# Kernel optimization log

Hardware: AMD Instinct MI355X
Metric: run time of the kernel (lower is better)

## Reference

```python
import jax, jax.numpy as jnp
import numpy as np

B, S, H, V, A = 64, 512, 1024, 32000, 16
MAX_LEN = 2 * 512 + 2  # 2*TEST_SEQ_LENGTH + 2


def setup_inputs() -> dict:
    key = jax.random.key(0)
    ks = jax.random.split(key, 8)
    sc_h = 1.0 / np.sqrt(H)
    return {
        "x": jax.random.randint(ks[0], (B, S), 0, V),
        "true_actions": jax.random.randint(ks[1], (B, S), 0, A),
        "true_states": jax.random.randint(ks[2], (B, S), 0, A),
        "use_forcing": 0,
        "embed_tok": jax.random.normal(ks[3], (V, H), jnp.float32) * 0.02,
        "embed_pos": jax.random.normal(ks[4], (MAX_LEN, H), jnp.float32) * 0.02,
        "Wi": jax.random.normal(ks[5], (H, 4 * H), jnp.float32) * sc_h,
        "Wh": jax.random.normal(ks[6], (H, 4 * H), jnp.float32) * sc_h,
        "bh": jnp.zeros((4 * H,), jnp.float32),
        "Wd": jax.random.normal(ks[7], (H, A), jnp.float32) * sc_h,
        "bd": jnp.zeros((A,), jnp.float32),
    }


def reference(x, true_actions, true_states, use_forcing,
              embed_tok, embed_pos, Wi, Wh, bh, Wd, bd):
    batch, seq = x.shape
    # token + positional embedding
    xe = embed_tok[x] + embed_pos[jnp.arange(seq)][None, :, :]  # [B,S,H]
    # precompute input contribution to all gates (hoisted out of the scan)
    xi = jnp.einsum('bsh,hg->bsg', xe, Wi)  # [B,S,4H]

    def step(carry, xt):
        c, h = carry
        z = xt + h @ Wh + bh                      # [B,4H]
        i, f, g, o = jnp.split(z, 4, axis=-1)     # flax gate order i,f,g,o
        c = jax.nn.sigmoid(f) * c + jax.nn.sigmoid(i) * jnp.tanh(g)
        h = jax.nn.sigmoid(o) * jnp.tanh(c)
        return (c, h), h

    c0 = jnp.zeros((batch, H), xi.dtype)
    h0 = jnp.zeros((batch, H), xi.dtype)
    _, hs = jax.lax.scan(step, (c0, h0), jnp.swapaxes(xi, 0, 1))  # [S,B,H]
    hs = jnp.swapaxes(hs, 0, 1)  # [B,S,H]

    logits_buf = hs @ Wd + bd  # [B,S,A]
    dummy = jnp.zeros((batch, seq, 1), logits_buf.dtype)
    return (dummy, logits_buf, dummy)
```

## Files before the change

kernel.cpp:

```cpp
#include <hip/hip_runtime.h>
#include <hip/hip_bf16.h>

#define BB 64
#define SS 512
#define HH 1024
#define G4 4096

using bf8_t = __attribute__((ext_vector_type(8))) short;
using f32x4 = __attribute__((ext_vector_type(4))) float;
typedef unsigned long long ull;

__device__ inline ushort f2bf(float f) {
  __hip_bfloat16 h = __float2bfloat16(f);
  return *reinterpret_cast<ushort*>(&h);
}
__device__ inline float bf2f(ushort u) {
  unsigned v = ((unsigned)u) << 16;
  return __uint_as_float(v);
}

__global__ __launch_bounds__(256) void k_transpose_cast(
    const float* __restrict__ in, ushort* __restrict__ out, int R, int C) {
  __shared__ float tile[32][33];
  int c0 = blockIdx.x * 32, r0 = blockIdx.y * 32;
  int tx = threadIdx.x & 31, ty = threadIdx.x >> 5;
  for (int i = ty; i < 32; i += 8) {
    int r = r0 + i, c = c0 + tx;
    tile[i][tx] = (r < R && c < C) ? in[(size_t)r * C + c] : 0.f;
  }
  __syncthreads();
  for (int i = ty; i < 32; i += 8) {
    int c = c0 + i, r = r0 + tx;
    if (c < C && r < R) out[(size_t)c * R + r] = f2bf(tile[tx][i]);
  }
}

__global__ __launch_bounds__(256) void k_embed(
    const int* __restrict__ x, const float* __restrict__ etok,
    const float* __restrict__ epos, ushort* __restrict__ Ae) {
  int row = blockIdx.x;
  int t = row >> 6, b = row & 63;
  int tok = x[b * SS + t];
  const float4* tp = (const float4*)(etok + (size_t)tok * HH);
  const float4* pp = (const float4*)(epos + (size_t)t * HH);
  int i = threadIdx.x;
  float4 a = tp[i], p = pp[i];
  ushort4 r = make_ushort4(f2bf(a.x + p.x), f2bf(a.y + p.y),
                           f2bf(a.z + p.z), f2bf(a.w + p.w));
  ((ushort4*)(Ae + (size_t)row * HH))[i] = r;
}

__global__ __launch_bounds__(256) void k_gemm_xi(
    const ushort* __restrict__ Ag, const ushort* __restrict__ Bt,
    const float* __restrict__ bias, ushort* __restrict__ Cout, int N) {
  __shared__ alignas(16) ushort As[128 * 40];
  __shared__ alignas(16) ushort Bs[128 * 40];
  const int m0 = blockIdx.y * 128, n0 = blockIdx.x * 128;
  const int tid = threadIdx.x;
  const int srow = tid >> 1, shalf = tid & 1;
  const int w = tid >> 6, lane = tid & 63;
  const int wm = w >> 1, wn = w & 1;
  const int lr = lane & 15, kq = lane >> 4;
  f32x4 acc[4][4] = {};
  for (int k0 = 0; k0 < HH; k0 += 32) {
    const uint4* ga = (const uint4*)(Ag + (size_t)(m0 + srow) * HH + k0 + shalf * 16);
    const uint4* gb = (const uint4*)(Bt + (size_t)(n0 + srow) * HH + k0 + shalf * 16);
    uint4 va0 = ga[0], va1 = ga[1];
    uint4 vb0 = gb[0], vb1 = gb[1];
    __syncthreads();
    *(uint4*)&As[srow * 40 + shalf * 16]     = va0;
    *(uint4*)&As[srow * 40 + shalf * 16 + 8] = va1;
    *(uint4*)&Bs[srow * 40 + shalf * 16]     = vb0;
    *(uint4*)&Bs[srow * 40 + shalf * 16 + 8] = vb1;
    __syncthreads();
    bf8_t fa[4], fb[4];
#pragma unroll
    for (int i = 0; i < 4; ++i) {
      fa[i] = *(const bf8_t*)&As[(wm * 64 + i * 16 + lr) * 40 + kq * 8];
      fb[i] = *(const bf8_t*)&Bs[(wn * 64 + i * 16 + lr) * 40 + kq * 8];
    }
#pragma unroll
    for (int mi = 0; mi < 4; ++mi)
#pragma unroll
      for (int ni = 0; ni < 4; ++ni)
        acc[mi][ni] = __builtin_amdgcn_mfma_f32_16x16x32_bf16(fa[mi], fb[ni], acc[mi][ni], 0, 0, 0);
  }
#pragma unroll
  for (int mi = 0; mi < 4; ++mi) {
    int grow = m0 + wm * 64 + mi * 16 + kq * 4;
#pragma unroll
    for (int ni = 0; ni < 4; ++ni) {
      int gcol = n0 + wn * 64 + ni * 16 + lr;
      float bv = bias[gcol];
#pragma unroll
      for (int r = 0; r < 4; ++r)
        Cout[(size_t)(grow + r) * N + gcol] = f2bf(acc[mi][ni][r] + bv);
    }
  }
}

__global__ __launch_bounds__(256, 1) void k_recur(
    const ushort* __restrict__ Wh_t,
    const ushort* __restrict__ xi,
    ushort* __restrict__ hs,
    uint4* __restrict__ fragA) {
  __shared__ alignas(16) ushort htile[2048 * 8];
  __shared__ ushort hxch[4][16][4];
  const ull SENT = 0x7F7F7F7F7F7F7F7FULL;
  const int grp = blockIdx.x >> 6;
  const int mem = blockIdx.x & 63;
  const int n0 = mem * 16;
  const int brow0 = grp * 16;
  const int tid = threadIdx.x;
  const int w = tid >> 6, lane = tid & 63;
  const int lr = lane & 15, kq = lane >> 4;
  const int gate = lr >> 2;
  const int c0 = n0 + 4 * w;
  const int col = c0 + (lr & 3);
  const int gc = gate * 1024 + col;

  bf8_t fbr[32];
  {
    const ushort* wrow = Wh_t + (size_t)gc * HH + kq * 8;
#pragma unroll
    for (int k = 0; k < 32; ++k)
      asm volatile("global_load_dwordx4 %0, %1, off offset:%c2"
                   : "=v"(fbr[k]) : "v"(wrow), "i"(k * 64));
    asm volatile("s_waitcnt vmcnt(0)" ::: "memory");
  }

  const int pk0 = c0 >> 5, pq = (c0 >> 3) & 3;
  const int pboff = (c0 & 7) * 2;

  float cr[4] = {0.f, 0.f, 0.f, 0.f};

  ushort xv[4];
  {
    const ushort* xr = xi + ((size_t)brow0 + kq * 4) * G4 + gc;
#pragma unroll
    for (int r = 0; r < 4; ++r) xv[r] = xr[(size_t)r * G4];
  }

  for (int t = 0; t < SS; ++t) {
    ull uvv[16];
    if (t == 0) {
#pragma unroll
      for (int j = 0; j < 16; ++j) uvv[j] = 0;
    } else {
      const ull* q = (const ull*)(fragA + ((size_t)(t - 1) * 4 + grp) * 2048);
      bool again;
      do {
#pragma unroll
        for (int i = 0; i < 8; ++i) {
          uvv[2 * i]     = __hip_atomic_load(q + 2 * tid + 512 * i,
                              __ATOMIC_RELAXED, __HIP_MEMORY_SCOPE_AGENT);
          uvv[2 * i + 1] = __hip_atomic_load(q + 2 * tid + 512 * i + 1,
                              __ATOMIC_RELAXED, __HIP_MEMORY_SCOPE_AGENT);
        }
        again = false;
#pragma unroll
        for (int j = 0; j < 16; ++j) again |= (uvv[j] == SENT);
      } while (again);
    }
    __syncthreads();

#pragma unroll
    for (int i = 0; i < 8; ++i) {
      uint4 sw;
      sw.x = (unsigned)uvv[2 * i];     sw.y = (unsigned)(uvv[2 * i] >> 32);
      sw.z = (unsigned)uvv[2 * i + 1]; sw.w = (unsigned)(uvv[2 * i + 1] >> 32);
      *(uint4*)&htile[(size_t)(tid + 256 * i) * 8] = sw;
    }
    __syncthreads();

    ushort xn[4];
    {
      int tn = (t + 1 < SS) ? t + 1 : t;
      const ushort* xr = xi + ((size_t)tn * 64 + brow0 + kq * 4) * G4 + gc;
#pragma unroll
      for (int r = 0; r < 4; ++r) xn[r] = xr[(size_t)r * G4];
    }

    f32x4 acc0 = {}, acc1 = {};
#pragma unroll
    for (int k = 0; k < 32; k += 2) {
      bf8_t fa0 = *(const bf8_t*)&htile[(k * 64 + lane) * 8];
      bf8_t fa1 = *(const bf8_t*)&htile[((k + 1) * 64 + lane) * 8];
      acc0 = __builtin_amdgcn_mfma_f32_16x16x32_bf16(fa0, fbr[k], acc0, 0, 0, 0);
      acc1 = __builtin_amdgcn_mfma_f32_16x16x32_bf16(fa1, fbr[k + 1], acc1, 0, 0, 0);
    }

    float z[4], zb[4], zc[4], zd[4];
#pragma unroll
    for (int r = 0; r < 4; ++r) z[r] = acc0[r] + acc1[r] + bf2f(xv[r]);
#pragma unroll
    for (int r = 0; r < 4; ++r) {
      zb[r] = __shfl_xor(z[r], 4);
      zc[r] = __shfl_xor(z[r], 8);
      zd[r] = __shfl_xor(zb[r], 8);
    }
    ushort hvals[4];
#pragma unroll
    for (int r = 0; r < 4; ++r) {
      float zi = gate == 0 ? z[r] : gate == 1 ? zb[r] : gate == 2 ? zc[r] : zd[r];
      float zf = gate == 0 ? zb[r] : gate == 1 ? z[r] : gate == 2 ? zd[r] : zc[r];
      float zg = gate == 0 ? zc[r] : gate == 1 ? zd[r] : gate == 2 ? z[r] : zb[r];
      float zo = gate == 0 ? zd[r] : gate == 1 ? zc[r] : gate == 2 ? zb[r] : z[r];
      float si = 1.f / (1.f + __expf(-zi));
      float sf = 1.f / (1.f + __expf(-zf));
      float so = 1.f / (1.f + __expf(-zo));
      float tg = 1.f - 2.f / (1.f + __expf(2.f * zg));
      float c  = sf * cr[r] + si * tg;
      cr[r] = c;
      float tc = 1.f - 2.f / (1.f + __expf(2.f * c));
      hvals[r] = f2bf(so * tc);
    }
    if (lr < 4) {
#pragma unroll
      for (int r = 0; r < 4; ++r) hxch[w][kq * 4 + r][lr] = hvals[r];
    }
    if (lane < 16) {
      uint2 ho8 = *(const uint2*)&hxch[w][lane][0];
      ull val = ((ull)ho8.y << 32) | ho8.x;
      char* fbase = (char*)(fragA + ((size_t)t * 4 + grp) * 2048);
      ull* fdst = (ull*)(fbase + (size_t)(pk0 * 64 + pq * 16 + lane) * 16 + pboff);
      __hip_atomic_exchange(fdst, val, __ATOMIC_RELAXED,
                            __HIP_MEMORY_SCOPE_AGENT);
      *(uint2*)(hs + ((size_t)(t + 1) * 64 + brow0 + lane) * HH + c0) = ho8;
    }
    xv[0] = xn[0]; xv[1] = xn[1]; xv[2] = xn[2]; xv[3] = xn[3];
  }
}

__global__ __launch_bounds__(256) void k_logits(
    const ushort* __restrict__ hs1, const ushort* __restrict__ Wdt,
    const float* __restrict__ bd, float* __restrict__ out) {
  int gid = blockIdx.x * 256 + threadIdx.x;
  int a = gid & 15, row = gid >> 4;
  int t = row >> 6, b = row & 63;
  const uint4* hp = (const uint4*)(hs1 + (size_t)row * HH);
  const uint4* wp = (const uint4*)(Wdt + (size_t)a * HH);
  float sum = 0.f;
#pragma unroll 4
  for (int i = 0; i < HH / 8; ++i) {
    uint4 hv = hp[i], wv = wp[i];
    const uint* hu = (const uint*)&hv;
    const uint* wu = (const uint*)&wv;
#pragma unroll
    for (int j = 0; j < 4; ++j) {
      sum += bf2f((ushort)(hu[j] & 0xffff)) * bf2f((ushort)(wu[j] & 0xffff));
      sum += bf2f((ushort)(hu[j] >> 16)) * bf2f((ushort)(wu[j] >> 16));
    }
  }
  out[32768 + ((size_t)b * SS + t) * 16 + a] = sum + bd[a];
}

extern "C" void kernel_launch(void* const* d_in, const int* in_sizes, int n_in,
                              void* d_out, int out_size, void* d_ws, size_t ws_size,
                              hipStream_t stream) {
  const int*   x    = (const int*)d_in[0];
  const float* etok = (const float*)d_in[4];
  const float* epos = (const float*)d_in[5];
  const float* Wi   = (const float*)d_in[6];
  const float* Wh   = (const float*)d_in[7];
  const float* bh   = (const float*)d_in[8];
  const float* Wd   = (const float*)d_in[9];
  const float* bd   = (const float*)d_in[10];

  char* ws = (char*)d_ws;
  size_t off = 0;
  ushort* Wi_t = (ushort*)(ws + off); off += (size_t)G4 * HH * 2;
  ushort* Wh_t = (ushort*)(ws + off); off += (size_t)G4 * HH * 2;
  ushort* Wd_t = (ushort*)(ws + off); off += 65536;
  char* AeFrag = ws + off;            off += (size_t)512 * 4 * 2048 * 16;
  ushort* Ae   = (ushort*)AeFrag;
  uint4*  fragA = (uint4*)AeFrag;
  ushort* xi   = (ushort*)(ws + off); off += (size_t)BB * SS * G4 * 2;
  ushort* hs   = (ushort*)(ws + off); off += (size_t)(SS + 1) * BB * HH * 2;

  hipMemsetAsync(d_out, 0, (size_t)out_size * 4, stream);

  dim3 b256(256);
  k_transpose_cast<<<dim3(G4 / 32, HH / 32), b256, 0, stream>>>(Wi, Wi_t, HH, G4);
  k_transpose_cast<<<dim3(G4 / 32, HH / 32), b256, 0, stream>>>(Wh, Wh_t, HH, G4);
  k_transpose_cast<<<dim3(1, HH / 32), b256, 0, stream>>>(Wd, Wd_t, HH, 16);
  k_embed<<<BB * SS, b256, 0, stream>>>(x, etok, epos, Ae);
  k_gemm_xi<<<dim3(G4 / 128, BB * SS / 128), b256, 0, stream>>>(Ae, Wi_t, bh, xi, G4);
  hipMemsetAsync(fragA, 0x7F, (size_t)512 * 4 * 2048 * 16, stream);
  k_recur<<<256, b256, 0, stream>>>(Wh_t, xi, hs, fragA);
  k_logits<<<BB * SS * 16 / 256, b256, 0, stream>>>(hs + (size_t)BB * HH, Wd_t, bd,
                                                    (float*)d_out);
}
```

Before: 2.839 ms.

## Replace sentinel polling with per-block step counters in LSTM recurrence

The recurrence kernel no longer spins on the whole h fragment until no sentinel values remain. Each block now publishes a per-step counter after its exchange writes drain, one wave polls the 64 counters of its group, and the fragment is then read with ordinary loads. This also drops the large 0x7F memset of the exchange buffer and moves the next xi prefetch to after publishing. The cost is an extra barrier, a vmcnt drain and a token store per step. The plain reads rely on relaxed atomics and waitcnt ordering rather than explicit release/acquire fences, which may be a memory-ordering risk.

```diff
diff --git a/kernel.cpp b/kernel.cpp
--- a/kernel.cpp
+++ b/kernel.cpp
@@ -103,10 +103,10 @@
     const ushort* __restrict__ Wh_t,
     const ushort* __restrict__ xi,
     ushort* __restrict__ hs,
-    uint4* __restrict__ fragA) {
+    uint4* __restrict__ fragA,
+    unsigned* __restrict__ tokens) {
   __shared__ alignas(16) ushort htile[2048 * 8];
   __shared__ ushort hxch[4][16][4];
-  const ull SENT = 0x7F7F7F7F7F7F7F7FULL;
   const int grp = blockIdx.x >> 6;
   const int mem = blockIdx.x & 63;
   const int n0 = mem * 16;
@@ -116,8 +116,8 @@
   const int lr = lane & 15, kq = lane >> 4;
   const int gate = lr >> 2;
   const int c0 = n0 + 4 * w;
-  const int col = c0 + (lr & 3);
-  const int gc = gate * 1024 + col;
+  const int gc = gate * 1024 + c0 + (lr & 3);
+  unsigned* gtok = tokens + grp * 64;
 
   bf8_t fbr[32];
   {
@@ -142,44 +142,29 @@
   }
 
   for (int t = 0; t < SS; ++t) {
-    ull uvv[16];
+    uint4 hv[8];
     if (t == 0) {
 #pragma unroll
-      for (int j = 0; j < 16; ++j) uvv[j] = 0;
+      for (int i = 0; i < 8; ++i) hv[i] = uint4{0, 0, 0, 0};
     } else {
-      const ull* q = (const ull*)(fragA + ((size_t)(t - 1) * 4 + grp) * 2048);
-      bool again;
-      do {
-#pragma unroll
-        for (int i = 0; i < 8; ++i) {
-          uvv[2 * i]     = __hip_atomic_load(q + 2 * tid + 512 * i,
-                              __ATOMIC_RELAXED, __HIP_MEMORY_SCOPE_AGENT);
-          uvv[2 * i + 1] = __hip_atomic_load(q + 2 * tid + 512 * i + 1,
-                              __ATOMIC_RELAXED, __HIP_MEMORY_SCOPE_AGENT);
-        }
-        again = false;
-#pragma unroll
-        for (int j = 0; j < 16; ++j) again |= (uvv[j] == SENT);
-      } while (again);
-    }
+      if (w == 0) {
+        bool ok;
+        do {
+          unsigned v = __hip_atomic_load(gtok + lane, __ATOMIC_RELAXED,
+                                         __HIP_MEMORY_SCOPE_AGENT);
+          ok = __all(v >= (unsigned)t);
+        } while (!ok);
+      }
+      __syncthreads();
+      const uint4* src = fragA + ((size_t)(t - 1) * 4 + grp) * 2048;
+#pragma unroll
+      for (int i = 0; i < 8; ++i) hv[i] = src[tid + 256 * i];
+    }
+
+#pragma unroll
+    for (int i = 0; i < 8; ++i)
+      *(uint4*)&htile[(size_t)(tid + 256 * i) * 8] = hv[i];
     __syncthreads();
-
-#pragma unroll
-    for (int i = 0; i < 8; ++i) {
-      uint4 sw;
-      sw.x = (unsigned)uvv[2 * i];     sw.y = (unsigned)(uvv[2 * i] >> 32);
-      sw.z = (unsigned)uvv[2 * i + 1]; sw.w = (unsigned)(uvv[2 * i + 1] >> 32);
-      *(uint4*)&htile[(size_t)(tid + 256 * i) * 8] = sw;
-    }
-    __syncthreads();
-
-    ushort xn[4];
-    {
-      int tn = (t + 1 < SS) ? t + 1 : t;
-      const ushort* xr = xi + ((size_t)tn * 64 + brow0 + kq * 4) * G4 + gc;
-#pragma unroll
-      for (int r = 0; r < 4; ++r) xn[r] = xr[(size_t)r * G4];
-    }
 
     f32x4 acc0 = {}, acc1 = {};
 #pragma unroll
@@ -219,16 +204,32 @@
 #pragma unroll
       for (int r = 0; r < 4; ++r) hxch[w][kq * 4 + r][lr] = hvals[r];
     }
-    if (lane < 16) {
-      uint2 ho8 = *(const uint2*)&hxch[w][lane][0];
-      ull val = ((ull)ho8.y << 32) | ho8.x;
-      char* fbase = (char*)(fragA + ((size_t)t * 4 + grp) * 2048);
-      ull* fdst = (ull*)(fbase + (size_t)(pk0 * 64 + pq * 16 + lane) * 16 + pboff);
-      __hip_atomic_exchange(fdst, val, __ATOMIC_RELAXED,
-                            __HIP_MEMORY_SCOPE_AGENT);
+    uint2 ho8 = {0, 0};
+    if (lane < 16) ho8 = *(const uint2*)&hxch[w][lane][0];
+
+    if (t + 1 < SS) {
+      if (lane < 16) {
+        ull val = ((ull)ho8.y << 32) | ho8.x;
+        char* fbase = (char*)(fragA + ((size_t)t * 4 + grp) * 2048);
+        ull* fdst = (ull*)(fbase + (size_t)(pk0 * 64 + pq * 16 + lane) * 16 + pboff);
+        ull old = __hip_atomic_exchange(fdst, val, __ATOMIC_RELAXED,
+                                        __HIP_MEMORY_SCOPE_AGENT);
+        asm volatile("" :: "v"(old));
+      }
+      asm volatile("s_waitcnt vmcnt(0)" ::: "memory");
+      __syncthreads();
+      if (tid == 0)
+        __hip_atomic_store(gtok + mem, (unsigned)(t + 1), __ATOMIC_RELAXED,
+                           __HIP_MEMORY_SCOPE_AGENT);
+    }
+    if (lane < 16)
       *(uint2*)(hs + ((size_t)(t + 1) * 64 + brow0 + lane) * HH + c0) = ho8;
-    }
-    xv[0] = xn[0]; xv[1] = xn[1]; xv[2] = xn[2]; xv[3] = xn[3];
+    {
+      int tn = (t + 1 < SS) ? t + 1 : t;
+      const ushort* xr = xi + ((size_t)tn * 64 + brow0 + kq * 4) * G4 + gc;
+#pragma unroll
+      for (int r = 0; r < 4; ++r) xv[r] = xr[(size_t)r * G4];
+    }
   }
 }
 
@@ -277,8 +278,10 @@
   uint4*  fragA = (uint4*)AeFrag;
   ushort* xi   = (ushort*)(ws + off); off += (size_t)BB * SS * G4 * 2;
   ushort* hs   = (ushort*)(ws + off); off += (size_t)(SS + 1) * BB * HH * 2;
+  unsigned* tokens = (unsigned*)(ws + off); off += 4 * 64 * 4;
 
   hipMemsetAsync(d_out, 0, (size_t)out_size * 4, stream);
+  hipMemsetAsync(tokens, 0, 4 * 64 * 4, stream);
 
   dim3 b256(256);
   k_transpose_cast<<<dim3(G4 / 32, HH / 32), b256, 0, stream>>>(Wi, Wi_t, HH, G4);
@@ -286,8 +289,7 @@
   k_transpose_cast<<<dim3(1, HH / 32), b256, 0, stream>>>(Wd, Wd_t, HH, 16);
   k_embed<<<BB * SS, b256, 0, stream>>>(x, etok, epos, Ae);
   k_gemm_xi<<<dim3(G4 / 128, BB * SS / 128), b256, 0, stream>>>(Ae, Wi_t, bh, xi, G4);
-  hipMemsetAsync(fragA, 0x7F, (size_t)512 * 4 * 2048 * 16, stream);
-  k_recur<<<256, b256, 0, stream>>>(Wh_t, xi, hs, fragA);
+  k_recur<<<256, b256, 0, stream>>>(Wh_t, xi, hs, fragA, tokens);
   k_logits<<<BB * SS * 16 / 256, b256, 0, stream>>>(hs + (size_t)BB * HH, Wd_t, bd,
                                                     (float*)d_out);
 }
```

After: 3.432 ms. +20.9%, slower.
